# Optimization experiments

Measured on AMD Instinct MI355X. Metric: run time of the kernel, lower is better.

The kernel has to match this reference:

```python
import jax, jax.numpy as jnp
import numpy as np

B, S, DM, DC = 16, 4096, 1280, 768
N_AOE, N_IMG, N_DELTA = 16, 16, 16
ANAT_GATE, DIS_GATE, DELTA_SCALE = 0.5, 0.5, 1.0


def setup_inputs() -> dict:
    key = jax.random.key(0)
    ks = jax.random.split(key, 9)
    def lin(k, fan_in, fan_out):
        return jax.random.normal(k, (fan_in, fan_out), jnp.float32) / np.sqrt(fan_in)
    return {
        "hidden_states": jax.random.normal(ks[0], (B, S, DM), jnp.float32),
        "encoder_hidden_states": jax.random.normal(ks[1], (B, N_AOE + N_IMG + N_DELTA, DC), jnp.float32),
        "w_q": lin(ks[2], DM, DM),
        "w_k": lin(ks[3], DC, DM),
        "w_v": lin(ks[4], DC, DM),
        "w_k_dis": lin(ks[5], DC, DM),
        "w_v_dis": lin(ks[6], DC, DM),
        "w_out": lin(ks[7], DM, DM),
        "b_out": jnp.zeros((DM,), jnp.float32),
        "n_heads": 8,
    }


def _heads(x, h):
    b, s, d = x.shape
    return x.reshape(b, s, h, d // h).transpose(0, 2, 1, 3)  # [B,H,S,dh]


def _attend(q, k, v, scale):
    # q:[B,H,Sq,dh], k/v:[B,H,Sk,dh], Sk small (16)
    scores = jnp.einsum("bhqd,bhkd->bhqk", q, k) * scale
    probs = jax.nn.softmax(scores, axis=-1)
    return jnp.einsum("bhqk,bhkd->bhqd", probs, v)


def reference(hidden_states, encoder_hidden_states, w_q, w_k, w_v,
              w_k_dis, w_v_dis, w_out, b_out, n_heads):
    residual = hidden_states
    dh = DM // n_heads
    scale = 1.0 / np.sqrt(dh)

    dis_tok = encoder_hidden_states[:, :N_AOE, :]
    anat_tok = encoder_hidden_states[:, N_AOE:N_AOE + N_IMG, :]
    delta_tok = encoder_hidden_states[:, -N_DELTA:, :]

    q = _heads(hidden_states @ w_q, n_heads)
    z_anat = _attend(q, _heads(anat_tok @ w_k, n_heads), _heads(anat_tok @ w_v, n_heads), scale)
    z_dis = _attend(q, _heads(dis_tok @ w_k_dis, n_heads), _heads(dis_tok @ w_v_dis, n_heads), scale)
    z_delta = _attend(q, _heads(delta_tok @ w_k_dis, n_heads), _heads(delta_tok @ w_v_dis, n_heads), scale)

    z = ANAT_GATE * z_anat + DIS_GATE * z_dis + DELTA_SCALE * z_delta
    out = z.transpose(0, 2, 1, 3).reshape(hidden_states.shape[0], -1, DM)
    out = out @ w_out + b_out  # to_out[0]; to_out[1] dropout = identity in eval
    return out + residual  # residual_connection, rescale_output_factor=1.0
```

## Files before the change

### kernel.cpp

```cpp
#include <hip/hip_runtime.h>
#include <hip/hip_bf16.h>

#define B_ 16
#define S_ 4096
#define DM_ 1280
#define DC_ 768
#define NC_ 384
#define SCALE_ 0.07905694150420949f

typedef __attribute__((ext_vector_type(8))) short bf16x8;
typedef __attribute__((ext_vector_type(4))) float f32x4;
typedef __attribute__((ext_vector_type(4))) unsigned short u16x4;

#define S_BARRIER() asm volatile("s_barrier" ::: "memory")
#define WAIT_VM(n) asm volatile("s_waitcnt vmcnt(" #n ")" ::: "memory")
#define WAIT_LGKM0() asm volatile("s_waitcnt lgkmcnt(0)" ::: "memory")

__device__ __forceinline__ unsigned short f2bf(float f) {
    unsigned int u = __builtin_bit_cast(unsigned int, f);
    u = (u + 0x7FFFu + ((u >> 16) & 1u)) >> 16;
    return (unsigned short)u;
}

__device__ __forceinline__ bf16x8 pack8(float4 x0, float4 x1) {
    bf16x8 a;
    a[0] = __builtin_bit_cast(short, __float2bfloat16(x0.x));
    a[1] = __builtin_bit_cast(short, __float2bfloat16(x0.y));
    a[2] = __builtin_bit_cast(short, __float2bfloat16(x0.z));
    a[3] = __builtin_bit_cast(short, __float2bfloat16(x0.w));
    a[4] = __builtin_bit_cast(short, __float2bfloat16(x1.x));
    a[5] = __builtin_bit_cast(short, __float2bfloat16(x1.y));
    a[6] = __builtin_bit_cast(short, __float2bfloat16(x1.z));
    a[7] = __builtin_bit_cast(short, __float2bfloat16(x1.w));
    return a;
}

__device__ __forceinline__ void gload16(const void* g, void* l) {
    __builtin_amdgcn_global_load_lds(
        (const __attribute__((address_space(1))) void*)g,
        (__attribute__((address_space(3))) void*)l, 16, 0, 0);
}

__device__ __forceinline__ void tcvt_body(const float* __restrict__ in,
                                          unsigned short* __restrict__ out,
                                          int R, int C, int bx, int by, int tid) {
    __shared__ float tile[32][33];
    int c0 = bx * 32, r0 = by * 32;
    int tx = tid & 31, ty = tid >> 5;
    for (int i = ty; i < 32; i += 8)
        tile[i][tx] = in[(size_t)(r0 + i) * C + c0 + tx];
    __syncthreads();
    for (int i = ty; i < 32; i += 8)
        out[(size_t)(c0 + i) * R + r0 + tx] = f2bf(tile[tx][i]);
}

__global__ __launch_bounds__(256)
void k_prep(const float* __restrict__ wq, const float* __restrict__ wk,
            const float* __restrict__ wv, const float* __restrict__ wkd,
            const float* __restrict__ wvd, const float* __restrict__ wout,
            unsigned short* __restrict__ wq_bf, unsigned short* __restrict__ wTk,
            unsigned short* __restrict__ wTv, unsigned short* __restrict__ wTkd,
            unsigned short* __restrict__ wTvd, unsigned short* __restrict__ woutT) {
    int bid = blockIdx.x, tid = threadIdx.x;
    if (bid < 1600) {
        int i = bid * 256 + tid;
        float4 v = ((const float4*)wq)[i];
        u16x4 o = { f2bf(v.x), f2bf(v.y), f2bf(v.z), f2bf(v.w) };
        ((u16x4*)wq_bf)[i] = o;
    } else if (bid < 2560) {
        int r = bid - 1600; tcvt_body(wk,  wTk,  DC_, DM_, r % 40, r / 40, tid);
    } else if (bid < 3520) {
        int r = bid - 2560; tcvt_body(wv,  wTv,  DC_, DM_, r % 40, r / 40, tid);
    } else if (bid < 4480) {
        int r = bid - 3520; tcvt_body(wkd, wTkd, DC_, DM_, r % 40, r / 40, tid);
    } else if (bid < 5440) {
        int r = bid - 4480; tcvt_body(wvd, wTvd, DC_, DM_, r % 40, r / 40, tid);
    } else {
        int r = bid - 5440; tcvt_body(wout, woutT, DM_, DM_, r % 40, r / 40, tid);
    }
}

__global__ __launch_bounds__(256)
void k_au2(const float* __restrict__ enc,
           const unsigned short* __restrict__ wTk, const unsigned short* __restrict__ wTv,
           const unsigned short* __restrict__ wTkd, const unsigned short* __restrict__ wTvd,
           const unsigned short* __restrict__ wqbf, const unsigned short* __restrict__ woutT,
           unsigned short* __restrict__ At2, unsigned short* __restrict__ Ut2) {
    __shared__ unsigned short kvLds[16 * 168];
    int bid0 = blockIdx.x;
    bool isA = bid0 < 384;
    int bid = isA ? bid0 : bid0 - 384;
    int b = bid & 15, r_ = bid >> 4, x = r_ >> 3, h = r_ & 7;
    int tid = threadIdx.x, w = tid >> 6, l = tid & 63, l15 = l & 15, l4 = l >> 4;
    int xh = x * 8 + h;
    int tok0 = (x == 0) ? 16 : ((x == 1) ? 0 : 32);
    const unsigned short* wTproj = isA ? ((x == 0) ? wTk : wTkd)
                                       : ((x == 0) ? wTv : wTvd);
    const unsigned short* wmat = isA ? wqbf : woutT;
    float postscale = isA ? SCALE_ : ((x == 2) ? 1.0f : 0.5f);
    f32x4 zero = {0.f, 0.f, 0.f, 0.f};

    {
        const float* ap = enc + ((size_t)(b * 48 + tok0 + l15)) * DC_;
        f32x4 pacc[3];
        #pragma unroll
        for (int i = 0; i < 3; i++) pacc[i] = zero;
        for (int kk = 0; kk < 24; kk++) {
            const float4* hp = (const float4*)(ap + kk * 32 + l4 * 8);
            bf16x8 af = pack8(hp[0], hp[1]);
            int i = 0;
            for (int t2 = w; t2 < 10; t2 += 4, i++) {
                int n0 = h * 160 + t2 * 16;
                bf16x8 bf = *(const bf16x8*)(wTproj + (size_t)(n0 + l15) * DC_ + kk * 32 + l4 * 8);
                pacc[i] = __builtin_amdgcn_mfma_f32_16x16x32_bf16(af, bf, pacc[i], 0, 0, 0);
            }
        }
        int i = 0;
        for (int t2 = w; t2 < 10; t2 += 4, i++) {
            #pragma unroll
            for (int r = 0; r < 4; r++)
                kvLds[(l4 * 4 + r) * 168 + t2 * 16 + l15] = f2bf(pacc[i][r]);
        }
    }
    __syncthreads();

    bf16x8 bfr[5];
    #pragma unroll
    for (int kk = 0; kk < 5; kk++)
        bfr[kk] = *(const bf16x8*)&kvLds[l15 * 168 + kk * 32 + l4 * 8];

    for (int tt = 0; tt < 20; tt++) {
        int d0 = w * 320 + tt * 16;
        f32x4 acc = zero;
        if (isA) {
            #pragma unroll
            for (int kk = 0; kk < 5; kk++) {
                bf16x8 af = *(const bf16x8*)(wmat + (size_t)(d0 + l15) * DM_ + h * 160 + kk * 32 + l4 * 8);
                acc = __builtin_amdgcn_mfma_f32_16x16x32_bf16(af, bfr[kk], acc, 0, 0, 0);
            }
            int c = xh * 16 + l15;
            u16x4 pk;
            #pragma unroll
            for (int r = 0; r < 4; r++) pk[r] = f2bf(acc[r] * postscale);
            *(u16x4*)(At2 + ((size_t)(b * 40 + (d0 >> 5)) * NC_ + c) * 32 + (d0 & 31) + l4 * 4) = pk;
        } else {
            #pragma unroll
            for (int kk = 0; kk < 5; kk++) {
                bf16x8 af = *(const bf16x8*)(wmat + (size_t)(d0 + l15) * DM_ + h * 160 + kk * 32 + l4 * 8);
                acc = __builtin_amdgcn_mfma_f32_16x16x32_bf16(bfr[kk], af, acc, 0, 0, 0);
            }
            int e = d0 + l15;
            u16x4 pk;
            #pragma unroll
            for (int r = 0; r < 4; r++) pk[r] = f2bf(acc[r] * postscale);
            *(u16x4*)(Ut2 + ((size_t)(b * 12 + (xh >> 1)) * DM_ + e) * 32 + (xh & 1) * 16 + l4 * 4) = pk;
        }
    }
}

__global__ __launch_bounds__(256, 2)
void k_fused2(const float* __restrict__ hid, const unsigned short* __restrict__ At2,
              const unsigned short* __restrict__ Ut2, const float* __restrict__ bo,
              float* __restrict__ out) {
    __shared__ char smem[73728];
    unsigned short* Apnl = (unsigned short*)smem;
    char* Hlds = smem + 49152;
    int bid = blockIdx.x;
    int orig = (bid & 7) * 128 + (bid >> 3);
    int b = orig >> 6, st = orig & 63;
    int s0 = st * 64;
    int tid = threadIdx.x, w = tid >> 6, l = tid & 63, l15 = l & 15, l4 = l >> 4;
    int rdsw = (l4 ^ ((l15 >> 1) & 3)) * 8;
    const unsigned short* Ab = At2 + (size_t)b * 40 * NC_ * 32;
    const float* hsrc = hid + ((size_t)b * S_ + s0) * DM_;
    f32x4 zero = {0.f, 0.f, 0.f, 0.f};

    uint4 pf4[12];

    {
        f32x4 acc[24];
        #pragma unroll
        for (int g = 0; g < 24; g++) acc[g] = zero;

        auto stageA = [&](int kk, int ab) {
            const unsigned short* slab = Ab + (size_t)kk * (NC_ * 32);
            #pragma unroll
            for (int i = 0; i < 6; i++) {
                int idx = i * 256 + tid;
                int c = idx >> 2, m = (idx & 3) ^ ((c >> 1) & 3);
                gload16(slab + (size_t)c * 32 + m * 8, smem + ab * 24576 + idx * 16);
            }
        };
        auto stageH = [&](int kk, int hb) {
            #pragma unroll
            for (int i = 0; i < 2; i++) {
                int idx = i * 256 + tid;
                int r = idx >> 3, sg = (idx & 7) ^ (r & 7);
                gload16(hsrc + (size_t)r * DM_ + kk * 32 + sg * 4, Hlds + hb * 8192 + idx * 16);
            }
        };
        auto compute = [&](int ab, int hb) {
            int r = w * 16 + l15;
            float4 lo = *(const float4*)(Hlds + hb * 8192 + r * 128 + (((2 * l4) ^ (l15 & 7)) * 16));
            float4 hi = *(const float4*)(Hlds + hb * 8192 + r * 128 + (((2 * l4 + 1) ^ (l15 & 7)) * 16));
            bf16x8 hpk = pack8(lo, hi);
            __builtin_amdgcn_s_setprio(1);
            #pragma unroll
            for (int g = 0; g < 24; g++) {
                bf16x8 af = *(const bf16x8*)&Apnl[ab * 12288 + (g * 16 + l15) * 32 + rdsw];
                acc[g] = __builtin_amdgcn_mfma_f32_16x16x32_bf16(af, hpk, acc[g], 0, 0, 0);
            }
            __builtin_amdgcn_s_setprio(0);
        };
        auto SITER = [&](int kk) {
            stageA(kk + 1, (kk + 1) & 1);
            stageH(kk + 2, (kk + 2) % 3);
            WAIT_VM(10);
            S_BARRIER();
            compute(kk & 1, kk % 3);
            WAIT_LGKM0();
            S_BARRIER();
        };

        stageA(0, 0); stageH(0, 0); stageH(1, 1);
        for (int k0 = 0; k0 < 36; k0 += 6) {
            SITER(k0 + 0); SITER(k0 + 1); SITER(k0 + 2);
            SITER(k0 + 3); SITER(k0 + 4); SITER(k0 + 5);
        }
        SITER(36); SITER(37);
        stageA(39, 1);
        WAIT_VM(8);
        S_BARRIER();
        compute(0, 38 % 3);
        WAIT_LGKM0();
        S_BARRIER();
        WAIT_VM(0);
        S_BARRIER();
        compute(1, 39 % 3);
        WAIT_LGKM0();
        S_BARRIER();

        unsigned int Wp[24][2];
        #pragma unroll
        for (int g = 0; g < 24; g++) {
            float v0 = acc[g][0], v1 = acc[g][1], v2 = acc[g][2], v3 = acc[g][3];
            float mx = fmaxf(fmaxf(v0, v1), fmaxf(v2, v3));
            mx = fmaxf(mx, __shfl_xor(mx, 16));
            mx = fmaxf(mx, __shfl_xor(mx, 32));
            float e0 = __expf(v0 - mx), e1 = __expf(v1 - mx), e2 = __expf(v2 - mx), e3 = __expf(v3 - mx);
            float sm = e0 + e1 + e2 + e3;
            sm += __shfl_xor(sm, 16);
            sm += __shfl_xor(sm, 32);
            float rs = 1.0f / sm;
            Wp[g][0] = (unsigned int)f2bf(e0 * rs) | ((unsigned int)f2bf(e1 * rs) << 16);
            Wp[g][1] = (unsigned int)f2bf(e2 * rs) | ((unsigned int)f2bf(e3 * rs) << 16);
        }
        int srcA = (((2 * l4) & 3) << 4) | l15;
        int srcB = (((2 * l4 + 1) & 3) << 4) | l15;
        bool hiG = (l4 >= 2);
        #pragma unroll
        for (int K = 0; K < 12; K++) {
            int g0 = 2 * K, g1 = 2 * K + 1;
            unsigned int a0 = (unsigned int)__shfl((int)Wp[g0][0], srcA);
            unsigned int a1 = (unsigned int)__shfl((int)Wp[g0][1], srcA);
            unsigned int b0 = (unsigned int)__shfl((int)Wp[g0][0], srcB);
            unsigned int b1 = (unsigned int)__shfl((int)Wp[g0][1], srcB);
            unsigned int c0 = (unsigned int)__shfl((int)Wp[g1][0], srcA);
            unsigned int c1 = (unsigned int)__shfl((int)Wp[g1][1], srcA);
            unsigned int d0 = (unsigned int)__shfl((int)Wp[g1][0], srcB);
            unsigned int d1 = (unsigned int)__shfl((int)Wp[g1][1], srcB);
            uint4 fr;
            fr.x = hiG ? c0 : a0;
            fr.y = hiG ? c1 : a1;
            fr.z = hiG ? d0 : b0;
            fr.w = hiG ? d1 : b1;
            pf4[K] = fr;
        }
    }
    __syncthreads();

    const unsigned short* Ub = Ut2 + (size_t)b * 12 * DM_ * 32;
    unsigned short* Usm = (unsigned short*)smem;
    int srow = s0 + w * 16 + l15;

    for (int ecb = 0; ecb < 20; ecb++) {
        #pragma unroll
        for (int kk2 = 0; kk2 < 12; kk2++) {
            const unsigned short* slab = Ub + ((size_t)kk2 * DM_ + ecb * 64) * 32;
            int r = tid >> 2, m = (tid & 3) ^ ((r >> 1) & 3);
            gload16(slab + (size_t)r * 32 + m * 8, smem + kk2 * 4096 + tid * 16);
        }
        WAIT_VM(0);
        S_BARRIER();

        f32x4 acc2[4];
        #pragma unroll
        for (int ej = 0; ej < 4; ej++) acc2[ej] = zero;
        __builtin_amdgcn_s_setprio(1);
        #pragma unroll
        for (int kk2 = 0; kk2 < 12; kk2++) {
            bf16x8 pfr = __builtin_bit_cast(bf16x8, pf4[kk2]);
            #pragma unroll
            for (int ej = 0; ej < 4; ej++) {
                bf16x8 uf = *(const bf16x8*)&Usm[kk2 * 2048 + (ej * 16 + l15) * 32 + rdsw];
                acc2[ej] = __builtin_amdgcn_mfma_f32_16x16x32_bf16(uf, pfr, acc2[ej], 0, 0, 0);
            }
        }
        __builtin_amdgcn_s_setprio(0);
        WAIT_LGKM0();
        S_BARRIER();

        #pragma unroll
        for (int ej = 0; ej < 4; ej++) {
            int e0c = ecb * 64 + ej * 16 + l4 * 4;
            float4 b4 = *(const float4*)(bo + e0c);
            size_t off = ((size_t)b * S_ + srow) * DM_ + e0c;
            float4 h4 = *(const float4*)(hid + off);
            f32x4 a = acc2[ej];
            float4 o4;
            o4.x = a[0] + b4.x + h4.x;
            o4.y = a[1] + b4.y + h4.y;
            o4.z = a[2] + b4.z + h4.z;
            o4.w = a[3] + b4.w + h4.w;
            *(float4*)(out + off) = o4;
        }
    }
}

extern "C" void kernel_launch(void* const* d_in, const int* in_sizes, int n_in,
                              void* d_out, int out_size, void* d_ws, size_t ws_size,
                              hipStream_t stream) {
    const float* hid  = (const float*)d_in[0];
    const float* enc  = (const float*)d_in[1];
    const float* wq   = (const float*)d_in[2];
    const float* wk   = (const float*)d_in[3];
    const float* wv   = (const float*)d_in[4];
    const float* wkd  = (const float*)d_in[5];
    const float* wvd  = (const float*)d_in[6];
    const float* wout = (const float*)d_in[7];
    const float* bo   = (const float*)d_in[8];
    float* out = (float*)d_out;

    char* ws = (char*)d_ws;
    unsigned short* At2    = (unsigned short*)(ws);
    unsigned short* Ut2    = (unsigned short*)(ws + 15728640);
    unsigned short* wq_bf  = (unsigned short*)(ws + 31457280);
    unsigned short* woutT  = (unsigned short*)(ws + 34734080);
    unsigned short* wTk    = (unsigned short*)(ws + 38010880);
    unsigned short* wTv    = (unsigned short*)(ws + 39976960);
    unsigned short* wTkd   = (unsigned short*)(ws + 41943040);
    unsigned short* wTvd   = (unsigned short*)(ws + 43909120);

    k_prep<<<7040, 256, 0, stream>>>(wq, wk, wv, wkd, wvd, wout,
                                     wq_bf, wTk, wTv, wTkd, wTvd, woutT);
    k_au2<<<768, 256, 0, stream>>>(enc, wTk, wTv, wTkd, wTvd, wq_bf, woutT, At2, Ut2);
    k_fused2<<<1024, 256, 0, stream>>>(hid, At2, Ut2, bo, out);
}
```

Before: 395.0 us.

## Load score-phase operands directly from global memory instead of LDS pipeline

The first (score) phase of the fused kernel drops its LDS staging of the A panel and hidden rows with async loads and barriers. Each lane now reads its MFMA fragments straight from global memory. LDS shrinks to 48KB and the launch bound rises to 3 blocks per CU to raise occupancy and remove barrier stalls. Softmax is moved inside the shuffle loop to cut register pressure. The risk is that A-panel data is now fetched redundantly by each of the four waves and load latency is exposed without explicit prefetching.

Result: slower. 692.0 us (+75.2%).

```diff
diff --git a/kernel.cpp b/kernel.cpp
--- a/kernel.cpp
+++ b/kernel.cpp
@@ -158,21 +158,17 @@
     }
 }
 
-__global__ __launch_bounds__(256, 2)
-void k_fused2(const float* __restrict__ hid, const unsigned short* __restrict__ At2,
+__global__ __launch_bounds__(256, 3)
+void k_fused3(const float* __restrict__ hid, const unsigned short* __restrict__ At2,
               const unsigned short* __restrict__ Ut2, const float* __restrict__ bo,
               float* __restrict__ out) {
-    __shared__ char smem[73728];
-    unsigned short* Apnl = (unsigned short*)smem;
-    char* Hlds = smem + 49152;
+    __shared__ char smem[49152];
     int bid = blockIdx.x;
     int orig = (bid & 7) * 128 + (bid >> 3);
     int b = orig >> 6, st = orig & 63;
     int s0 = st * 64;
     int tid = threadIdx.x, w = tid >> 6, l = tid & 63, l15 = l & 15, l4 = l >> 4;
     int rdsw = (l4 ^ ((l15 >> 1) & 3)) * 8;
-    const unsigned short* Ab = At2 + (size_t)b * 40 * NC_ * 32;
-    const float* hsrc = hid + ((size_t)b * S_ + s0) * DM_;
     f32x4 zero = {0.f, 0.f, 0.f, 0.f};
 
     uint4 pf4[12];
@@ -182,93 +178,49 @@
         #pragma unroll
         for (int g = 0; g < 24; g++) acc[g] = zero;
 
-        auto stageA = [&](int kk, int ab) {
-            const unsigned short* slab = Ab + (size_t)kk * (NC_ * 32);
-            #pragma unroll
-            for (int i = 0; i < 6; i++) {
-                int idx = i * 256 + tid;
-                int c = idx >> 2, m = (idx & 3) ^ ((c >> 1) & 3);
-                gload16(slab + (size_t)c * 32 + m * 8, smem + ab * 24576 + idx * 16);
-            }
-        };
-        auto stageH = [&](int kk, int hb) {
-            #pragma unroll
-            for (int i = 0; i < 2; i++) {
-                int idx = i * 256 + tid;
-                int r = idx >> 3, sg = (idx & 7) ^ (r & 7);
-                gload16(hsrc + (size_t)r * DM_ + kk * 32 + sg * 4, Hlds + hb * 8192 + idx * 16);
-            }
-        };
-        auto compute = [&](int ab, int hb) {
-            int r = w * 16 + l15;
-            float4 lo = *(const float4*)(Hlds + hb * 8192 + r * 128 + (((2 * l4) ^ (l15 & 7)) * 16));
-            float4 hi = *(const float4*)(Hlds + hb * 8192 + r * 128 + (((2 * l4 + 1) ^ (l15 & 7)) * 16));
-            bf16x8 hpk = pack8(lo, hi);
-            __builtin_amdgcn_s_setprio(1);
+        const unsigned short* Afr = At2 + (size_t)b * 40 * NC_ * 32 + l15 * 32 + l4 * 8;
+        const float* hrow = hid + ((size_t)b * S_ + s0 + w * 16 + l15) * DM_ + l4 * 8;
+
+        for (int kk = 0; kk < 40; kk++) {
+            const float4* hp = (const float4*)(hrow + kk * 32);
+            bf16x8 hpk = pack8(hp[0], hp[1]);
+            const unsigned short* slab = Afr + (size_t)kk * (NC_ * 32);
             #pragma unroll
             for (int g = 0; g < 24; g++) {
-                bf16x8 af = *(const bf16x8*)&Apnl[ab * 12288 + (g * 16 + l15) * 32 + rdsw];
+                bf16x8 af = *(const bf16x8*)(slab + g * 512);
                 acc[g] = __builtin_amdgcn_mfma_f32_16x16x32_bf16(af, hpk, acc[g], 0, 0, 0);
             }
-            __builtin_amdgcn_s_setprio(0);
-        };
-        auto SITER = [&](int kk) {
-            stageA(kk + 1, (kk + 1) & 1);
-            stageH(kk + 2, (kk + 2) % 3);
-            WAIT_VM(10);
-            S_BARRIER();
-            compute(kk & 1, kk % 3);
-            WAIT_LGKM0();
-            S_BARRIER();
-        };
-
-        stageA(0, 0); stageH(0, 0); stageH(1, 1);
-        for (int k0 = 0; k0 < 36; k0 += 6) {
-            SITER(k0 + 0); SITER(k0 + 1); SITER(k0 + 2);
-            SITER(k0 + 3); SITER(k0 + 4); SITER(k0 + 5);
-        }
-        SITER(36); SITER(37);
-        stageA(39, 1);
-        WAIT_VM(8);
-        S_BARRIER();
-        compute(0, 38 % 3);
-        WAIT_LGKM0();
-        S_BARRIER();
-        WAIT_VM(0);
-        S_BARRIER();
-        compute(1, 39 % 3);
-        WAIT_LGKM0();
-        S_BARRIER();
-
-        unsigned int Wp[24][2];
-        #pragma unroll
-        for (int g = 0; g < 24; g++) {
-            float v0 = acc[g][0], v1 = acc[g][1], v2 = acc[g][2], v3 = acc[g][3];
-            float mx = fmaxf(fmaxf(v0, v1), fmaxf(v2, v3));
-            mx = fmaxf(mx, __shfl_xor(mx, 16));
-            mx = fmaxf(mx, __shfl_xor(mx, 32));
-            float e0 = __expf(v0 - mx), e1 = __expf(v1 - mx), e2 = __expf(v2 - mx), e3 = __expf(v3 - mx);
-            float sm = e0 + e1 + e2 + e3;
-            sm += __shfl_xor(sm, 16);
-            sm += __shfl_xor(sm, 32);
-            float rs = 1.0f / sm;
-            Wp[g][0] = (unsigned int)f2bf(e0 * rs) | ((unsigned int)f2bf(e1 * rs) << 16);
-            Wp[g][1] = (unsigned int)f2bf(e2 * rs) | ((unsigned int)f2bf(e3 * rs) << 16);
-        }
+        }
+
         int srcA = (((2 * l4) & 3) << 4) | l15;
         int srcB = (((2 * l4 + 1) & 3) << 4) | l15;
         bool hiG = (l4 >= 2);
         #pragma unroll
         for (int K = 0; K < 12; K++) {
-            int g0 = 2 * K, g1 = 2 * K + 1;
-            unsigned int a0 = (unsigned int)__shfl((int)Wp[g0][0], srcA);
-            unsigned int a1 = (unsigned int)__shfl((int)Wp[g0][1], srcA);
-            unsigned int b0 = (unsigned int)__shfl((int)Wp[g0][0], srcB);
-            unsigned int b1 = (unsigned int)__shfl((int)Wp[g0][1], srcB);
-            unsigned int c0 = (unsigned int)__shfl((int)Wp[g1][0], srcA);
-            unsigned int c1 = (unsigned int)__shfl((int)Wp[g1][1], srcA);
-            unsigned int d0 = (unsigned int)__shfl((int)Wp[g1][0], srcB);
-            unsigned int d1 = (unsigned int)__shfl((int)Wp[g1][1], srcB);
+            unsigned int Wg[2][2];
+            #pragma unroll
+            for (int t = 0; t < 2; t++) {
+                f32x4 a = acc[2 * K + t];
+                float v0 = a[0], v1 = a[1], v2 = a[2], v3 = a[3];
+                float mx = fmaxf(fmaxf(v0, v1), fmaxf(v2, v3));
+                mx = fmaxf(mx, __shfl_xor(mx, 16));
+                mx = fmaxf(mx, __shfl_xor(mx, 32));
+                float e0 = __expf(v0 - mx), e1 = __expf(v1 - mx), e2 = __expf(v2 - mx), e3 = __expf(v3 - mx);
+                float sm = e0 + e1 + e2 + e3;
+                sm += __shfl_xor(sm, 16);
+                sm += __shfl_xor(sm, 32);
+                float rs = 1.0f / sm;
+                Wg[t][0] = (unsigned int)f2bf(e0 * rs) | ((unsigned int)f2bf(e1 * rs) << 16);
+                Wg[t][1] = (unsigned int)f2bf(e2 * rs) | ((unsigned int)f2bf(e3 * rs) << 16);
+            }
+            unsigned int a0 = (unsigned int)__shfl((int)Wg[0][0], srcA);
+            unsigned int a1 = (unsigned int)__shfl((int)Wg[0][1], srcA);
+            unsigned int b0 = (unsigned int)__shfl((int)Wg[0][0], srcB);
+            unsigned int b1 = (unsigned int)__shfl((int)Wg[0][1], srcB);
+            unsigned int c0 = (unsigned int)__shfl((int)Wg[1][0], srcA);
+            unsigned int c1 = (unsigned int)__shfl((int)Wg[1][1], srcA);
+            unsigned int d0 = (unsigned int)__shfl((int)Wg[1][0], srcB);
+            unsigned int d1 = (unsigned int)__shfl((int)Wg[1][1], srcB);
             uint4 fr;
             fr.x = hiG ? c0 : a0;
             fr.y = hiG ? c1 : a1;
@@ -277,7 +229,6 @@
             pf4[K] = fr;
         }
     }
-    __syncthreads();
 
     const unsigned short* Ub = Ut2 + (size_t)b * 12 * DM_ * 32;
     unsigned short* Usm = (unsigned short*)smem;
@@ -354,5 +305,5 @@
     k_prep<<<7040, 256, 0, stream>>>(wq, wk, wv, wkd, wvd, wout,
                                      wq_bf, wTk, wTv, wTkd, wTvd, woutT);
     k_au2<<<768, 256, 0, stream>>>(enc, wTk, wTv, wTkd, wTvd, wq_bf, woutT, At2, Ut2);
-    k_fused2<<<1024, 256, 0, stream>>>(hid, At2, Ut2, bo, out);
-}
+    k_fused3<<<1024, 256, 0, stream>>>(hid, At2, Ut2, bo, out);
+}
```
